# Kernel tuning notes

Hardware: AMD Instinct MI355X
Metric: run time of the kernel (lower is better)

The kernel has to match this reference:

```python
import jax, jax.numpy as jnp
import numpy as np

# ThrusterLagConfig constants
PWM_CENTER = 7.5
PWM_HALF_RANGE = 2.5
DEADZONE = 0.05
SAT_GAIN = 2.0
TAU_INIT = 0.08
TAU_MIN = 0.01
DT = 0.01
N_THRUSTERS = 8


def setup_inputs() -> dict:
    key = jax.random.key(0)
    k_u, = jax.random.split(key, 1)
    B, L, C = 512, 8192, N_THRUSTERS
    # raw PWM duty in [5, 10]
    u_seq = jax.random.uniform(k_u, (B, L, C), dtype=jnp.float32, minval=5.0, maxval=10.0)
    # learnable tau parameter, initialized as in __init__:
    # tau0 = clamp(tau_init - tau_min, 1e-6); p0 = log(expm1(tau0))
    tau0 = max(TAU_INIT - TAU_MIN, 1e-6)
    p0 = float(np.log(np.expm1(tau0)))
    tau_param = jnp.full((C,), p0, dtype=jnp.float32)
    return {"u_seq": u_seq, "tau_param": tau_param}


def reference(u_seq, tau_param):
    # PWM duty -> [-1, 1]
    u_unit = (u_seq - PWM_CENTER) / PWM_HALF_RANGE
    # deadzone: softshrink(u, lambd) = sign(u) * max(|u| - lambd, 0)
    u_dz = jnp.sign(u_unit) * jnp.maximum(jnp.abs(u_unit) - DEADZONE, 0.0)
    # smooth saturation
    u_nl = jnp.tanh(SAT_GAIN * u_dz)  # (B, L, C)

    # a = exp(-dt / tau), tau = softplus(p) + tau_min, per channel (C,)
    tau = jax.nn.softplus(tau_param) + TAU_MIN
    a = jnp.exp(-DT / tau)  # (C,)

    # first-order lag IIR: u_eff[k] = a * u_eff[k-1] + (1 - a) * u_nl[k]
    # u0_eff defaults to u_nl[:, 0, :]
    u0 = u_nl[:, 0, :]  # (B, C)

    def step(u_prev, uk):
        u_new = a * u_prev + (1.0 - a) * uk
        return u_new, u_new

    xs = jnp.moveaxis(u_nl, 1, 0)  # (L, B, C)
    _, ys = jax.lax.scan(step, u0, xs)
    return jnp.moveaxis(ys, 0, 1)  # (B, L, C)
```

## Files before the change

kernel.cpp:

```cpp
#include <hip/hip_runtime.h>
#include <math.h>


typedef float v4f __attribute__((ext_vector_type(4)));

constexpr int kB     = 512;
constexpr int kL     = 8192;
constexpr int kC     = 8;
constexpr int kOut   = 512;
constexpr int kChunk = 128;
constexpr int kSegs  = kL / kOut;
constexpr int kNCh   = kOut / kChunk;

constexpr float kDT     = 0.01f;
constexpr float kTauMin = 0.01f;

__device__ __forceinline__ float rfl(float x) {
    return __int_as_float(__builtin_amdgcn_readfirstlane(__float_as_int(x)));
}

__device__ __forceinline__ float softplus_f(float p) {
    return fmaxf(p, 0.0f) + log1pf(__expf(-fabsf(p)));
}

__device__ __forceinline__ float u_nl(float u) {
    float s = fmaf(u, 0.8f, -6.0f);
    float m = fmaxf(fabsf(s) - 0.1f, 0.0f);
    float x = copysignf(m, s);
    float t = x * x;
    float p = fmaf(t, -0.0072811f, 0.070674f);
    p = fmaf(t, p, -0.297221f);
    p = fmaf(t, p, 0.996226f);
    return x * p;
}

template<int D>
__device__ __forceinline__ float dpp_shr(float v) {
    return __int_as_float(__builtin_amdgcn_update_dpp(
        0, __float_as_int(v), 0x110 | D, 0xF, 0xF, false));
}

__device__ __forceinline__ float bperm(int addr, float v) {
    return __int_as_float(__builtin_amdgcn_ds_bpermute(addr, __float_as_int(v)));
}

__global__ __launch_bounds__(256, 2) void scan_seg(const float* __restrict__ u,
                                                   const float* __restrict__ tp,
                                                   float* __restrict__ out) {
    const int lane = threadIdx.x & 63;
    const int seg  = blockIdx.x * 4 + (threadIdx.x >> 6);
    const int r    = seg >> 4;
    const int sq   = seg & (kSegs - 1);

    float a[kC], om[kC], a2[kC], a4[kC], a8[kC], a16[kC], ia2[kC], M[kC];
    float D[kC], W15[kC], W31[kC];
    #pragma unroll
    for (int c = 0; c < kC; ++c) {
        float tau = softplus_f(tp[c]) + kTauMin;
        float lna = -kDT / tau;
        float av  = __expf(lna);
        float v2 = av * av, v4 = v2 * v2, v8 = v4 * v4;
        a[c]   = rfl(av);
        om[c]  = rfl(1.0f - av);
        a2[c]  = rfl(v2);
        a4[c]  = rfl(v4);
        a8[c]  = rfl(v8);
        a16[c] = rfl(v8 * v8);
        ia2[c] = rfl(1.0f / v2);
        M[c]   = rfl(__expf(lna * (float)kChunk));
        D[c]   = __expf(lna * (float)(2 * lane));
        W15[c] = (lane & 16)  ? __expf(lna * (float)(2 * ((lane & 15) + 1))) : 0.0f;
        W31[c] = (lane >= 32) ? __expf(lna * (float)(2 * (lane - 31)))       : 0.0f;
    }

    const float* base  = u   + (size_t)r * kL * kC;
    float*       obase = out + (size_t)r * kL * kC;

    float K[kC];
    int start, nch, wfrom;
    if (sq == 0) {
        start = 0; nch = kNCh; wfrom = 0;
        v4f q0 = *(const v4f*)(base);
        v4f q1 = *(const v4f*)(base + 4);
        K[0] = u_nl(q0.x); K[1] = u_nl(q0.y); K[2] = u_nl(q0.z); K[3] = u_nl(q0.w);
        K[4] = u_nl(q1.x); K[5] = u_nl(q1.y); K[6] = u_nl(q1.z); K[7] = u_nl(q1.w);
    } else {
        start = sq * kOut - kChunk;
        nch = kNCh + 1; wfrom = 1;
        #pragma unroll
        for (int c = 0; c < kC; ++c) K[c] = 0.0f;
    }

    const int addr16 = ((lane & 48) - 1) << 2;
    const int addr31 = 31 << 2;
    const int addr63 = 63 << 2;

    const float* tb0 = base + (size_t)(start + lane * 2) * kC;
    v4f x0 = *(const v4f*)(tb0);
    v4f x1 = *(const v4f*)(tb0 + 4);
    v4f x2 = *(const v4f*)(tb0 + 8);
    v4f x3 = *(const v4f*)(tb0 + 12);

    for (int ch = 0; ch < nch; ++ch) {
        const size_t off = (size_t)(start + ch * kChunk + lane * 2) * kC;

        float l0[kC], l1[kC];
        #pragma unroll
        for (int c = 0; c < 4; ++c) {
            l0[c]     = om[c]     * u_nl(x0[c]);
            l0[c + 4] = om[c + 4] * u_nl(x1[c]);
            l1[c]     = fmaf(a[c],     l0[c],     om[c]     * u_nl(x2[c]));
            l1[c + 4] = fmaf(a[c + 4], l0[c + 4], om[c + 4] * u_nl(x3[c]));
        }

        if (ch + 1 < nch) {
            const float* nb = base + (off + (size_t)kChunk * kC);
            x0 = *(const v4f*)(nb);
            x1 = *(const v4f*)(nb + 4);
            x2 = *(const v4f*)(nb + 8);
            x3 = *(const v4f*)(nb + 12);
        }

        float I[kC];
        #pragma unroll
        for (int c = 0; c < kC; ++c) I[c] = l1[c];
        #pragma unroll
        for (int c = 0; c < kC; ++c) I[c] = fmaf(a2[c],  dpp_shr<1>(I[c]), I[c]);
        #pragma unroll
        for (int c = 0; c < kC; ++c) I[c] = fmaf(a4[c],  dpp_shr<2>(I[c]), I[c]);
        #pragma unroll
        for (int c = 0; c < kC; ++c) I[c] = fmaf(a8[c],  dpp_shr<4>(I[c]), I[c]);
        #pragma unroll
        for (int c = 0; c < kC; ++c) I[c] = fmaf(a16[c], dpp_shr<8>(I[c]), I[c]);
        #pragma unroll
        for (int c = 0; c < kC; ++c) I[c] = fmaf(W15[c], bperm(addr16, I[c]), I[c]);
        #pragma unroll
        for (int c = 0; c < kC; ++c) I[c] = fmaf(W31[c], bperm(addr31, I[c]), I[c]);

        float Tt[kC], E[kC];
        #pragma unroll
        for (int c = 0; c < kC; ++c) Tt[c] = bperm(addr63, I[c]);
        #pragma unroll
        for (int c = 0; c < kC; ++c) E[c] = (I[c] - l1[c]) * ia2[c];

        if (ch >= wfrom) {
            float* ob = obase + off;
            v4f y0a, y0b, y1a, y1b;
            #pragma unroll
            for (int c = 0; c < kC; ++c) {
                float C  = fmaf(D[c], K[c], E[c]);
                float cy = a[c] * C;
                float y0 = l0[c] + cy;
                float y1 = fmaf(a[c], cy, l1[c]);
                if (c < 4) { y0a[c] = y0; y1a[c] = y1; }
                else       { y0b[c - 4] = y0; y1b[c - 4] = y1; }
            }
            *(v4f*)(ob)      = y0a;
            *(v4f*)(ob + 4)  = y0b;
            *(v4f*)(ob + 8)  = y1a;
            *(v4f*)(ob + 12) = y1b;
        }

        #pragma unroll
        for (int c = 0; c < kC; ++c) K[c] = fmaf(M[c], K[c], Tt[c]);
    }
}

extern "C" void kernel_launch(void* const* d_in, const int* in_sizes, int n_in,
                              void* d_out, int out_size, void* d_ws, size_t ws_size,
                              hipStream_t stream) {
    const float* u  = (const float*)d_in[0];
    const float* tp = (const float*)d_in[1];
    float* out = (float*)d_out;

    scan_seg<<<(kB * kSegs) / 4, 256, 0, stream>>>(u, tp, out);
}
```

Baseline: 55.90 us.

## Use DPP row broadcasts for cross-row scan steps and vectorize elementwise math

Swaps the two ds_bpermute cross-row scan steps for DPP row_bcast15/row_bcast31 moves, so those steps no longer go through the LDS crossbar. Rewrites the deadzone as s minus clamp(s, ±0.1), which takes fewer ops than abs/max/copysign. Writes the elementwise nonlinearity, the chunk combine and the carry update with 4-wide vector types so the compiler can emit packed FP32 ops. This depends on the row_bcast DPP controls being supported on this GPU target; if they are not, the scan results would be wrong.

```diff
diff --git a/kernel.cpp b/kernel.cpp
--- a/kernel.cpp
+++ b/kernel.cpp
@@ -23,10 +23,25 @@
     return fmaxf(p, 0.0f) + log1pf(__expf(-fabsf(p)));
 }
 
-__device__ __forceinline__ float u_nl(float u) {
+__device__ __forceinline__ v4f u_nl4(v4f u) {
+    v4f s = u * 0.8f - 6.0f;
+    v4f x;
+    #pragma unroll
+    for (int i = 0; i < 4; ++i) {
+        float cl = fminf(fmaxf(s[i], -0.1f), 0.1f);
+        x[i] = s[i] - cl;
+    }
+    v4f t = x * x;
+    v4f p = t * -0.0072811f + 0.070674f;
+    p = t * p - 0.297221f;
+    p = t * p + 0.996226f;
+    return x * p;
+}
+
+__device__ __forceinline__ float u_nl1(float u) {
     float s = fmaf(u, 0.8f, -6.0f);
-    float m = fmaxf(fabsf(s) - 0.1f, 0.0f);
-    float x = copysignf(m, s);
+    float cl = fminf(fmaxf(s, -0.1f), 0.1f);
+    float x = s - cl;
     float t = x * x;
     float p = fmaf(t, -0.0072811f, 0.070674f);
     p = fmaf(t, p, -0.297221f);
@@ -34,11 +49,14 @@
     return x * p;
 }
 
-template<int D>
-__device__ __forceinline__ float dpp_shr(float v) {
+template<int CTRL>
+__device__ __forceinline__ float dpp_mov(float v) {
     return __int_as_float(__builtin_amdgcn_update_dpp(
-        0, __float_as_int(v), 0x110 | D, 0xF, 0xF, false));
-}
+        0, __float_as_int(v), CTRL, 0xF, 0xF, false));
+}
+#define DPP_SHR(d)   (0x110 | (d))
+#define DPP_BC15     0x142
+#define DPP_BC31     0x143
 
 __device__ __forceinline__ float bperm(int addr, float v) {
     return __int_as_float(__builtin_amdgcn_ds_bpermute(addr, __float_as_int(v)));
@@ -52,8 +70,9 @@
     const int r    = seg >> 4;
     const int sq   = seg & (kSegs - 1);
 
-    float a[kC], om[kC], a2[kC], a4[kC], a8[kC], a16[kC], ia2[kC], M[kC];
-    float D[kC], W15[kC], W31[kC];
+    float a[kC], a2[kC], a4[kC], a8[kC], a16[kC];
+    float om[kC], ia2[kC], Ms[kC];
+    v4f D0, D1, W15a, W15b, W31a, W31b;
     #pragma unroll
     for (int c = 0; c < kC; ++c) {
         float tau = softplus_f(tp[c]) + kTauMin;
@@ -67,32 +86,34 @@
         a8[c]  = rfl(v8);
         a16[c] = rfl(v8 * v8);
         ia2[c] = rfl(1.0f / v2);
-        M[c]   = rfl(__expf(lna * (float)kChunk));
-        D[c]   = __expf(lna * (float)(2 * lane));
-        W15[c] = (lane & 16)  ? __expf(lna * (float)(2 * ((lane & 15) + 1))) : 0.0f;
-        W31[c] = (lane >= 32) ? __expf(lna * (float)(2 * (lane - 31)))       : 0.0f;
-    }
+        Ms[c]  = rfl(__expf(lna * (float)kChunk));
+        float d   = __expf(lna * (float)(2 * lane));
+        float w15 = (lane & 16)  ? __expf(lna * (float)(2 * ((lane & 15) + 1))) : 0.0f;
+        float w31 = (lane >= 32) ? __expf(lna * (float)(2 * (lane - 31)))       : 0.0f;
+        if (c < 4) { D0[c] = d; W15a[c] = w15; W31a[c] = w31; }
+        else       { D1[c-4] = d; W15b[c-4] = w15; W31b[c-4] = w31; }
+    }
+    v4f A0 = {a[0],a[1],a[2],a[3]},    A1 = {a[4],a[5],a[6],a[7]};
+    v4f O0 = {om[0],om[1],om[2],om[3]}, O1 = {om[4],om[5],om[6],om[7]};
+    v4f V0 = {ia2[0],ia2[1],ia2[2],ia2[3]}, V1 = {ia2[4],ia2[5],ia2[6],ia2[7]};
+    v4f M0 = {Ms[0],Ms[1],Ms[2],Ms[3]}, M1 = {Ms[4],Ms[5],Ms[6],Ms[7]};
 
     const float* base  = u   + (size_t)r * kL * kC;
     float*       obase = out + (size_t)r * kL * kC;
 
-    float K[kC];
+    v4f K0, K1;
     int start, nch, wfrom;
     if (sq == 0) {
         start = 0; nch = kNCh; wfrom = 0;
-        v4f q0 = *(const v4f*)(base);
-        v4f q1 = *(const v4f*)(base + 4);
-        K[0] = u_nl(q0.x); K[1] = u_nl(q0.y); K[2] = u_nl(q0.z); K[3] = u_nl(q0.w);
-        K[4] = u_nl(q1.x); K[5] = u_nl(q1.y); K[6] = u_nl(q1.z); K[7] = u_nl(q1.w);
+        K0 = u_nl4(*(const v4f*)(base));
+        K1 = u_nl4(*(const v4f*)(base + 4));
     } else {
         start = sq * kOut - kChunk;
         nch = kNCh + 1; wfrom = 1;
-        #pragma unroll
-        for (int c = 0; c < kC; ++c) K[c] = 0.0f;
-    }
-
-    const int addr16 = ((lane & 48) - 1) << 2;
-    const int addr31 = 31 << 2;
+        K0 = (v4f){0,0,0,0};
+        K1 = (v4f){0,0,0,0};
+    }
+
     const int addr63 = 63 << 2;
 
     const float* tb0 = base + (size_t)(start + lane * 2) * kC;
@@ -104,14 +125,11 @@
     for (int ch = 0; ch < nch; ++ch) {
         const size_t off = (size_t)(start + ch * kChunk + lane * 2) * kC;
 
-        float l0[kC], l1[kC];
-        #pragma unroll
-        for (int c = 0; c < 4; ++c) {
-            l0[c]     = om[c]     * u_nl(x0[c]);
-            l0[c + 4] = om[c + 4] * u_nl(x1[c]);
-            l1[c]     = fmaf(a[c],     l0[c],     om[c]     * u_nl(x2[c]));
-            l1[c + 4] = fmaf(a[c + 4], l0[c + 4], om[c + 4] * u_nl(x3[c]));
-        }
+        v4f n0 = u_nl4(x0), n1 = u_nl4(x1), n2 = u_nl4(x2), n3 = u_nl4(x3);
+        v4f l00 = O0 * n0;
+        v4f l01 = O1 * n1;
+        v4f l10 = A0 * l00 + O0 * n2;
+        v4f l11 = A1 * l01 + O1 * n3;
 
         if (ch + 1 < nch) {
             const float* nb = base + (off + (size_t)kChunk * kC);
@@ -123,46 +141,51 @@
 
         float I[kC];
         #pragma unroll
-        for (int c = 0; c < kC; ++c) I[c] = l1[c];
-        #pragma unroll
-        for (int c = 0; c < kC; ++c) I[c] = fmaf(a2[c],  dpp_shr<1>(I[c]), I[c]);
-        #pragma unroll
-        for (int c = 0; c < kC; ++c) I[c] = fmaf(a4[c],  dpp_shr<2>(I[c]), I[c]);
-        #pragma unroll
-        for (int c = 0; c < kC; ++c) I[c] = fmaf(a8[c],  dpp_shr<4>(I[c]), I[c]);
-        #pragma unroll
-        for (int c = 0; c < kC; ++c) I[c] = fmaf(a16[c], dpp_shr<8>(I[c]), I[c]);
-        #pragma unroll
-        for (int c = 0; c < kC; ++c) I[c] = fmaf(W15[c], bperm(addr16, I[c]), I[c]);
-        #pragma unroll
-        for (int c = 0; c < kC; ++c) I[c] = fmaf(W31[c], bperm(addr31, I[c]), I[c]);
-
-        float Tt[kC], E[kC];
-        #pragma unroll
-        for (int c = 0; c < kC; ++c) Tt[c] = bperm(addr63, I[c]);
-        #pragma unroll
-        for (int c = 0; c < kC; ++c) E[c] = (I[c] - l1[c]) * ia2[c];
+        for (int c = 0; c < 4; ++c) { I[c] = l10[c]; I[c + 4] = l11[c]; }
+        #pragma unroll
+        for (int c = 0; c < kC; ++c) I[c] = fmaf(a2[c],  dpp_mov<DPP_SHR(1)>(I[c]), I[c]);
+        #pragma unroll
+        for (int c = 0; c < kC; ++c) I[c] = fmaf(a4[c],  dpp_mov<DPP_SHR(2)>(I[c]), I[c]);
+        #pragma unroll
+        for (int c = 0; c < kC; ++c) I[c] = fmaf(a8[c],  dpp_mov<DPP_SHR(4)>(I[c]), I[c]);
+        #pragma unroll
+        for (int c = 0; c < kC; ++c) I[c] = fmaf(a16[c], dpp_mov<DPP_SHR(8)>(I[c]), I[c]);
+        #pragma unroll
+        for (int c = 0; c < 4; ++c) {
+            I[c]     = fmaf(W15a[c], dpp_mov<DPP_BC15>(I[c]),     I[c]);
+            I[c + 4] = fmaf(W15b[c], dpp_mov<DPP_BC15>(I[c + 4]), I[c + 4]);
+        }
+        #pragma unroll
+        for (int c = 0; c < 4; ++c) {
+            I[c]     = fmaf(W31a[c], dpp_mov<DPP_BC31>(I[c]),     I[c]);
+            I[c + 4] = fmaf(W31b[c], dpp_mov<DPP_BC31>(I[c + 4]), I[c + 4]);
+        }
+
+        v4f Tt0, Tt1;
+        #pragma unroll
+        for (int c = 0; c < 4; ++c) {
+            Tt0[c] = bperm(addr63, I[c]);
+            Tt1[c] = bperm(addr63, I[c + 4]);
+        }
+        v4f I0 = {I[0], I[1], I[2], I[3]};
+        v4f I1 = {I[4], I[5], I[6], I[7]};
+        v4f E0 = (I0 - l10) * V0;
+        v4f E1 = (I1 - l11) * V1;
 
         if (ch >= wfrom) {
             float* ob = obase + off;
-            v4f y0a, y0b, y1a, y1b;
-            #pragma unroll
-            for (int c = 0; c < kC; ++c) {
-                float C  = fmaf(D[c], K[c], E[c]);
-                float cy = a[c] * C;
-                float y0 = l0[c] + cy;
-                float y1 = fmaf(a[c], cy, l1[c]);
-                if (c < 4) { y0a[c] = y0; y1a[c] = y1; }
-                else       { y0b[c - 4] = y0; y1b[c - 4] = y1; }
-            }
-            *(v4f*)(ob)      = y0a;
-            *(v4f*)(ob + 4)  = y0b;
-            *(v4f*)(ob + 8)  = y1a;
-            *(v4f*)(ob + 12) = y1b;
-        }
-
-        #pragma unroll
-        for (int c = 0; c < kC; ++c) K[c] = fmaf(M[c], K[c], Tt[c]);
+            v4f C0  = D0 * K0 + E0;
+            v4f C1  = D1 * K1 + E1;
+            v4f cy0 = A0 * C0;
+            v4f cy1 = A1 * C1;
+            *(v4f*)(ob)      = l00 + cy0;
+            *(v4f*)(ob + 4)  = l01 + cy1;
+            *(v4f*)(ob + 8)  = A0 * cy0 + l10;
+            *(v4f*)(ob + 12) = A1 * cy1 + l11;
+        }
+
+        K0 = M0 * K0 + Tt0;
+        K1 = M1 * K1 + Tt1;
     }
 }
 
```

Result: no change. 55.41 us (-0.9%).
